# Kernel optimization log

Measured on AMD Instinct MI355X. Metric: run time of the kernel, lower is better.

## Reference

```python
import jax, jax.numpy as jnp
import numpy as np

B = 16384
I = 1024  # inputs_size
H = 1024  # hidden_size


def _linear_params(key, fan_in, fan_out):
    # torch nn.Linear default init: U(-1/sqrt(fan_in), 1/sqrt(fan_in))
    kw, kb = jax.random.split(key)
    bound = 1.0 / np.sqrt(fan_in)
    W = jax.random.uniform(kw, (fan_out, fan_in), jnp.float32, -bound, bound)
    b = jax.random.uniform(kb, (fan_out,), jnp.float32, -bound, bound)
    return W, b


def setup_inputs() -> dict:
    key = jax.random.key(0)
    ks = jax.random.split(key, 8)
    inp = {
        "input": jax.random.normal(ks[0], (B, I), jnp.float32),
        "hidden": jax.random.normal(ks[1], (B, H), jnp.float32),
    }
    names = ["r_i", "r_h", "z_i", "z_h", "n_i", "n_h"]
    fan_ins = [I, H, I, H, I, H]
    for name, fi, k in zip(names, fan_ins, ks[2:]):
        W, b = _linear_params(k, fi, H)
        inp[f"W_{name}"] = W
        inp[f"b_{name}"] = b
    return inp


def reference(input, hidden,
              W_r_i, b_r_i, W_r_h, b_r_h,
              W_z_i, b_z_i, W_z_h, b_z_h,
              W_n_i, b_n_i, W_n_h, b_n_h):
    # Faithful to the original (including its bug: z uses r_layer_h(hidden)).
    r_h = hidden @ W_r_h.T + b_r_h  # reused by both r and z gates
    r = jax.nn.sigmoid(input @ W_r_i.T + b_r_i + r_h)
    z = jax.nn.sigmoid(input @ W_z_i.T + b_z_i + r_h)
    n = jnp.tanh(input @ W_n_i.T + b_n_i + r * (hidden @ W_n_h.T + b_n_h))
    next_hidden = (1.0 - z) * n + z * hidden
    return (next_hidden, next_hidden)
```

## Files before the change

### kernel.cpp

```cpp
#include <hip/hip_runtime.h>


#define BM 128
#define BN 64
#define BK 32

typedef __attribute__((ext_vector_type(8))) short          bf16x8;
typedef __attribute__((ext_vector_type(8))) unsigned short u16x8;
typedef __attribute__((ext_vector_type(4))) float          f32x4;

__device__ __forceinline__ unsigned short f2bf(float f) {
    union { float f; unsigned u; } v; v.f = f;
    unsigned r = v.u + 0x7FFFu + ((v.u >> 16) & 1u);
    return (unsigned short)(r >> 16);
}

__global__ __launch_bounds__(256) void convert_bf16(
    const float* __restrict__ in0, const float* __restrict__ in1,
    const float* __restrict__ w0, const float* __restrict__ w1,
    const float* __restrict__ w2, const float* __restrict__ w3,
    const float* __restrict__ w4, unsigned short* __restrict__ ws)
{
    const long long e = ((long long)blockIdx.x * 256 + threadIdx.x) * 8;
    const float* src;
    if (e < 16777216LL) {
        src = in0 + e;
    } else if (e < 33554432LL) {
        src = in1 + (e - 16777216LL);
    } else {
        const long long t = e - 33554432LL;
        const int g = (int)(t >> 20);
        const long long within = t & 1048575LL;
        const float* w = (g == 0) ? w0 : (g == 1) ? w1 : (g == 2) ? w2 : (g == 3) ? w3 : w4;
        src = w + within;
    }
    const float4 a = *reinterpret_cast<const float4*>(src);
    const float4 b = *reinterpret_cast<const float4*>(src + 4);
    u16x8 o;
    o[0] = f2bf(a.x); o[1] = f2bf(a.y); o[2] = f2bf(a.z); o[3] = f2bf(a.w);
    o[4] = f2bf(b.x); o[5] = f2bf(b.y); o[6] = f2bf(b.z); o[7] = f2bf(b.w);
    *reinterpret_cast<u16x8*>(ws + e) = o;
}

__device__ __forceinline__ void async16(const void* g, void* l) {
    __builtin_amdgcn_global_load_lds(
        (const __attribute__((address_space(1))) unsigned int*)g,
        (__attribute__((address_space(3))) unsigned int*)l, 16, 0, 0);
}

__global__ __launch_bounds__(256, 2) void gru_fused(
    const unsigned short* __restrict__ bf,
    const float* __restrict__ hidden,
    const float* __restrict__ b_ri, const float* __restrict__ b_rh,
    const float* __restrict__ b_zi, const float* __restrict__ b_ni,
    const float* __restrict__ b_nh,
    float* __restrict__ out)
{
    const int H = 1024, K = 1024;
    const int BH = 16384 * 1024;

    __shared__ __align__(16) unsigned char sBuf[36864];

    const int tid  = threadIdx.x;
    const int wave = tid >> 6;
    const int lane = tid & 63;
    const int quad = lane >> 4;
    const int l16  = lane & 15;

    const int row0 = blockIdx.y * BM;
    const int col0 = blockIdx.x * BN;

    const unsigned short* inB  = bf;
    const unsigned short* hidB = bf + 16777216;
    const unsigned short* wB   = bf + 33554432;

    const unsigned short* srcbase[9];
    int ldsoff[9];
    #pragma unroll
    for (int j = 0; j < 9; ++j) {
        const int s = (j * 4 + wave) * 64 + lane;
        ldsoff[j] = s * 16;
        if (s < 512) {
            const int r = s >> 2;
            srcbase[j] = inB + (long long)(row0 + r) * K + (s & 3) * 8;
        } else if (s < 1024) {
            const int r = (s - 512) >> 2;
            srcbase[j] = hidB + (long long)(row0 + r) * K + (s & 3) * 8;
        } else {
            const int t = s - 1024;
            const int g = t >> 8;
            const int tt = t & 255;
            const int n = tt >> 2;
            srcbase[j] = wB + (long long)g * 1048576 + (long long)(col0 + n) * K + (tt & 3) * 8;
        }
    }

    f32x4 acc[5][2][4];
    #pragma unroll
    for (int g = 0; g < 5; ++g)
        #pragma unroll
        for (int mi = 0; mi < 2; ++mi)
            #pragma unroll
            for (int ni = 0; ni < 4; ++ni)
                acc[g][mi][ni] = (f32x4){0.f, 0.f, 0.f, 0.f};

    for (int k0 = 0; k0 < K; k0 += BK) {
        __syncthreads();
        #pragma unroll
        for (int j = 0; j < 9; ++j)
            async16(srcbase[j] + k0, sBuf + ldsoff[j]);
        __syncthreads();

        bf16x8 aIn[2], aHid[2];
        #pragma unroll
        for (int mi = 0; mi < 2; ++mi) {
            const int r = wave * 32 + mi * 16 + l16;
            aIn [mi] = *reinterpret_cast<const bf16x8*>(&sBuf[r * 64 + quad * 16]);
            aHid[mi] = *reinterpret_cast<const bf16x8*>(&sBuf[8192 + r * 64 + quad * 16]);
        }
        #pragma unroll
        for (int g = 0; g < 5; ++g) {
            #pragma unroll
            for (int ni = 0; ni < 4; ++ni) {
                const int n = ni * 16 + l16;
                const bf16x8 b = *reinterpret_cast<const bf16x8*>(
                    &sBuf[16384 + g * 4096 + n * 64 + quad * 16]);
                #pragma unroll
                for (int mi = 0; mi < 2; ++mi) {
                    const bf16x8 a = (g == 1 || g == 4) ? aHid[mi] : aIn[mi];
                    acc[g][mi][ni] = __builtin_amdgcn_mfma_f32_16x16x32_bf16(a, b, acc[g][mi][ni], 0, 0, 0);
                }
            }
        }
    }

    #pragma unroll
    for (int ni = 0; ni < 4; ++ni) {
        const int gcol = col0 + ni * 16 + l16;
        const float bri = b_ri[gcol], brh = b_rh[gcol], bzi = b_zi[gcol];
        const float bni = b_ni[gcol], bnh = b_nh[gcol];
        #pragma unroll
        for (int mi = 0; mi < 2; ++mi) {
            #pragma unroll
            for (int r4 = 0; r4 < 4; ++r4) {
                const int grow = row0 + wave * 32 + mi * 16 + quad * 4 + r4;
                const float g_ri = acc[0][mi][ni][r4];
                const float g_rh = acc[1][mi][ni][r4];
                const float g_zi = acc[2][mi][ni][r4];
                const float g_ni = acc[3][mi][ni][r4];
                const float g_nh = acc[4][mi][ni][r4];
                const float rh = g_rh + brh;
                const float rr = 1.f / (1.f + __expf(-(g_ri + bri + rh)));
                const float zz = 1.f / (1.f + __expf(-(g_zi + bzi + rh)));
                const float nn = tanhf(g_ni + bni + rr * (g_nh + bnh));
                const float h  = hidden[(long long)grow * H + gcol];
                const float o  = (1.f - zz) * nn + zz * h;
                out[(long long)grow * H + gcol]      = o;
                out[BH + (long long)grow * H + gcol] = o;
            }
        }
    }
}

extern "C" void kernel_launch(void* const* d_in, const int* in_sizes, int n_in,
                              void* d_out, int out_size, void* d_ws, size_t ws_size,
                              hipStream_t stream) {
    const float* input  = (const float*)d_in[0];
    const float* hidden = (const float*)d_in[1];
    const float* W_ri = (const float*)d_in[2];
    const float* b_ri = (const float*)d_in[3];
    const float* W_rh = (const float*)d_in[4];
    const float* b_rh = (const float*)d_in[5];
    const float* W_zi = (const float*)d_in[6];
    const float* b_zi = (const float*)d_in[7];
    const float* W_ni = (const float*)d_in[10];
    const float* b_ni = (const float*)d_in[11];
    const float* W_nh = (const float*)d_in[12];
    const float* b_nh = (const float*)d_in[13];
    float* out = (float*)d_out;
    unsigned short* ws = (unsigned short*)d_ws;

    convert_bf16<<<18944, 256, 0, stream>>>(input, hidden, W_ri, W_rh, W_zi, W_ni, W_nh, ws);

    dim3 grid(1024 / BN, 16384 / BM);
    gru_fused<<<grid, 256, 0, stream>>>(ws, hidden, b_ri, b_rh, b_zi, b_ni, b_nh, out);
}
```

Baseline: 503.5 us.

## Double-buffer LDS tiles with XOR swizzle and grid-stride conversion kernel

The GEMM main loop now uses two LDS buffers, so the async global-to-LDS loads for the next K-slice are issued before computing on the current one. Partial vmcnt waits and raw barriers replace the full __syncthreads pairs. An XOR swizzle on the 16-byte chunk index is meant to reduce LDS bank conflicts on the fragment reads, and s_setprio raises wave priority during the MFMA block. The bf16 conversion kernel becomes a grid-stride loop with fewer blocks. Doubling LDS to 72KB per block may lower occupancy against the 2-blocks-per-CU launch bound.

Result: no change. 496.1 us (-1.5%).

```diff
diff --git a/kernel.cpp b/kernel.cpp
--- a/kernel.cpp
+++ b/kernel.cpp
@@ -4,6 +4,7 @@
 #define BM 128
 #define BN 64
 #define BK 32
+#define TILE_BYTES 36864
 
 typedef __attribute__((ext_vector_type(8))) short          bf16x8;
 typedef __attribute__((ext_vector_type(8))) unsigned short u16x8;
@@ -21,25 +22,29 @@
     const float* __restrict__ w2, const float* __restrict__ w3,
     const float* __restrict__ w4, unsigned short* __restrict__ ws)
 {
-    const long long e = ((long long)blockIdx.x * 256 + threadIdx.x) * 8;
-    const float* src;
-    if (e < 16777216LL) {
-        src = in0 + e;
-    } else if (e < 33554432LL) {
-        src = in1 + (e - 16777216LL);
-    } else {
-        const long long t = e - 33554432LL;
-        const int g = (int)(t >> 20);
-        const long long within = t & 1048575LL;
-        const float* w = (g == 0) ? w0 : (g == 1) ? w1 : (g == 2) ? w2 : (g == 3) ? w3 : w4;
-        src = w + within;
-    }
-    const float4 a = *reinterpret_cast<const float4*>(src);
-    const float4 b = *reinterpret_cast<const float4*>(src + 4);
-    u16x8 o;
-    o[0] = f2bf(a.x); o[1] = f2bf(a.y); o[2] = f2bf(a.z); o[3] = f2bf(a.w);
-    o[4] = f2bf(b.x); o[5] = f2bf(b.y); o[6] = f2bf(b.z); o[7] = f2bf(b.w);
-    *reinterpret_cast<u16x8*>(ws + e) = o;
+    const long long stride = (long long)gridDim.x * 256;
+    for (long long u = (long long)blockIdx.x * 256 + threadIdx.x;
+         u < 4849664LL; u += stride) {
+        const long long e = u * 8;
+        const float* src;
+        if (e < 16777216LL) {
+            src = in0 + e;
+        } else if (e < 33554432LL) {
+            src = in1 + (e - 16777216LL);
+        } else {
+            const long long t = e - 33554432LL;
+            const int g = (int)(t >> 20);
+            const long long within = t & 1048575LL;
+            const float* w = (g == 0) ? w0 : (g == 1) ? w1 : (g == 2) ? w2 : (g == 3) ? w3 : w4;
+            src = w + within;
+        }
+        const float4 a = *reinterpret_cast<const float4*>(src);
+        const float4 b = *reinterpret_cast<const float4*>(src + 4);
+        u16x8 o;
+        o[0] = f2bf(a.x); o[1] = f2bf(a.y); o[2] = f2bf(a.z); o[3] = f2bf(a.w);
+        o[4] = f2bf(b.x); o[5] = f2bf(b.y); o[6] = f2bf(b.z); o[7] = f2bf(b.w);
+        *reinterpret_cast<u16x8*>(ws + e) = o;
+    }
 }
 
 __device__ __forceinline__ void async16(const void* g, void* l) {
@@ -47,6 +52,8 @@
         (const __attribute__((address_space(1))) unsigned int*)g,
         (__attribute__((address_space(3))) unsigned int*)l, 16, 0, 0);
 }
+
+#define CFENCE() asm volatile("" ::: "memory")
 
 __global__ __launch_bounds__(256, 2) void gru_fused(
     const unsigned short* __restrict__ bf,
@@ -59,13 +66,14 @@
     const int H = 1024, K = 1024;
     const int BH = 16384 * 1024;
 
-    __shared__ __align__(16) unsigned char sBuf[36864];
+    __shared__ __align__(16) unsigned char sBuf[2][TILE_BYTES];
 
     const int tid  = threadIdx.x;
     const int wave = tid >> 6;
     const int lane = tid & 63;
     const int quad = lane >> 4;
     const int l16  = lane & 15;
+    const int sq   = quad ^ ((l16 >> 1) & 3);
 
     const int row0 = blockIdx.y * BM;
     const int col0 = blockIdx.x * BN;
@@ -82,16 +90,19 @@
         ldsoff[j] = s * 16;
         if (s < 512) {
             const int r = s >> 2;
-            srcbase[j] = inB + (long long)(row0 + r) * K + (s & 3) * 8;
+            const int c = (s & 3) ^ ((r >> 1) & 3);
+            srcbase[j] = inB + (long long)(row0 + r) * K + c * 8;
         } else if (s < 1024) {
             const int r = (s - 512) >> 2;
-            srcbase[j] = hidB + (long long)(row0 + r) * K + (s & 3) * 8;
+            const int c = (s & 3) ^ ((r >> 1) & 3);
+            srcbase[j] = hidB + (long long)(row0 + r) * K + c * 8;
         } else {
             const int t = s - 1024;
             const int g = t >> 8;
             const int tt = t & 255;
             const int n = tt >> 2;
-            srcbase[j] = wB + (long long)g * 1048576 + (long long)(col0 + n) * K + (tt & 3) * 8;
+            const int c = (tt & 3) ^ ((n >> 1) & 3);
+            srcbase[j] = wB + (long long)g * 1048576 + (long long)(col0 + n) * K + c * 8;
         }
     }
 
@@ -104,27 +115,31 @@
             for (int ni = 0; ni < 4; ++ni)
                 acc[g][mi][ni] = (f32x4){0.f, 0.f, 0.f, 0.f};
 
-    for (int k0 = 0; k0 < K; k0 += BK) {
-        __syncthreads();
+    unsigned char* b0 = &sBuf[0][0];
+    unsigned char* b1 = &sBuf[1][0];
+
+    auto stage = [&](int k0, unsigned char* dst) {
         #pragma unroll
         for (int j = 0; j < 9; ++j)
-            async16(srcbase[j] + k0, sBuf + ldsoff[j]);
-        __syncthreads();
-
+            async16(srcbase[j] + k0, dst + ldsoff[j]);
+    };
+
+    auto compute = [&](const unsigned char* sb) {
         bf16x8 aIn[2], aHid[2];
         #pragma unroll
         for (int mi = 0; mi < 2; ++mi) {
             const int r = wave * 32 + mi * 16 + l16;
-            aIn [mi] = *reinterpret_cast<const bf16x8*>(&sBuf[r * 64 + quad * 16]);
-            aHid[mi] = *reinterpret_cast<const bf16x8*>(&sBuf[8192 + r * 64 + quad * 16]);
-        }
+            aIn [mi] = *reinterpret_cast<const bf16x8*>(sb + r * 64 + sq * 16);
+            aHid[mi] = *reinterpret_cast<const bf16x8*>(sb + 8192 + r * 64 + sq * 16);
+        }
+        __builtin_amdgcn_s_setprio(1);
         #pragma unroll
         for (int g = 0; g < 5; ++g) {
             #pragma unroll
             for (int ni = 0; ni < 4; ++ni) {
                 const int n = ni * 16 + l16;
                 const bf16x8 b = *reinterpret_cast<const bf16x8*>(
-                    &sBuf[16384 + g * 4096 + n * 64 + quad * 16]);
+                    sb + 16384 + g * 4096 + n * 64 + sq * 16);
                 #pragma unroll
                 for (int mi = 0; mi < 2; ++mi) {
                     const bf16x8 a = (g == 1 || g == 4) ? aHid[mi] : aIn[mi];
@@ -132,7 +147,33 @@
                 }
             }
         }
-    }
+        __builtin_amdgcn_s_setprio(0);
+    };
+
+    stage(0, b0);
+    #pragma unroll 1
+    for (int i = 0; i < 15; ++i) {
+        const int k2 = i * 2 * BK;
+        stage(k2 + BK, b1);
+        asm volatile("s_waitcnt vmcnt(9)" ::: "memory");
+        __builtin_amdgcn_s_barrier(); CFENCE();
+        compute(b0); CFENCE();
+        __builtin_amdgcn_s_barrier(); CFENCE();
+
+        stage(k2 + 2 * BK, b0);
+        asm volatile("s_waitcnt vmcnt(9)" ::: "memory");
+        __builtin_amdgcn_s_barrier(); CFENCE();
+        compute(b1); CFENCE();
+        __builtin_amdgcn_s_barrier(); CFENCE();
+    }
+    stage(31 * BK, b1);
+    asm volatile("s_waitcnt vmcnt(9)" ::: "memory");
+    __builtin_amdgcn_s_barrier(); CFENCE();
+    compute(b0); CFENCE();
+    __builtin_amdgcn_s_barrier(); CFENCE();
+    asm volatile("s_waitcnt vmcnt(0)" ::: "memory");
+    __builtin_amdgcn_s_barrier(); CFENCE();
+    compute(b1);
 
     #pragma unroll
     for (int ni = 0; ni < 4; ++ni) {
@@ -180,7 +221,7 @@
     float* out = (float*)d_out;
     unsigned short* ws = (unsigned short*)d_ws;
 
-    convert_bf16<<<18944, 256, 0, stream>>>(input, hidden, W_ri, W_rh, W_zi, W_ni, W_nh, ws);
+    convert_bf16<<<2048, 256, 0, stream>>>(input, hidden, W_ri, W_rh, W_zi, W_ni, W_nh, ws);
 
     dim3 grid(1024 / BN, 16384 / BM);
     gru_fused<<<grid, 256, 0, stream>>>(ws, hidden, b_ri, b_rh, b_zi, b_ni, b_nh, out);
```
